# Performance work log

Hardware: AMD Instinct MI355X
Metric: run time of the kernel (lower is better)

Reference implementation:

```python
import jax, jax.numpy as jnp
import numpy as np

B, V, C1, C2 = 4, 256, 64, 32
H0, H1, H2, OUT = 128, 128, 256, 1


def setup_inputs() -> dict:
    key = jax.random.key(0)
    ks = jax.random.split(key, 16)
    init = lambda k, shape: (jax.random.normal(k, shape, jnp.float32) * 0.05)
    return {
        "adjacency": jax.random.randint(ks[0], (B, V, V), 0, 2, jnp.int32),
        "node_features": jax.random.normal(ks[1], (B, V, C1), jnp.float32),
        "edge_attributes": jax.random.normal(ks[2], (B, V, V, C2), jnp.float32),
        # EdgeConvE #1: MLP on concat(x_i, x_j - x_i, e_ij) -> H0 -> H0
        "ec1_W1": init(ks[3], (2 * C1 + C2, H0)), "ec1_b1": jnp.zeros((H0,), jnp.float32),
        "ec1_W2": init(ks[4], (H0, H0)), "ec1_b2": jnp.zeros((H0,), jnp.float32),
        # EdgeConvE #2: input features now H0-dim -> H1 -> H0
        "ec2_W1": init(ks[5], (2 * H0 + C2, H1)), "ec2_b1": jnp.zeros((H1,), jnp.float32),
        "ec2_W2": init(ks[6], (H1, H0)), "ec2_b2": jnp.zeros((H0,), jnp.float32),
        # pair-scoring MLP: Dense(H2, relu) -> Dense(1, sigmoid)
        "h3_W": init(ks[7], (2 * H0, H2)), "h3_b": jnp.zeros((H2,), jnp.float32),
        "out_W": init(ks[8], (H2, OUT)), "out_b": jnp.zeros((OUT,), jnp.float32),
    }


def _edge_conv_e(adj, x, e, W1, b1, W2, b2):
    # EdgeConv with edge attributes: msg_ij = MLP([x_i, x_j - x_i, e_ij]),
    # masked-max aggregation over neighbors j given by adjacency.
    Bv, Vn, C = x.shape
    xi = jnp.broadcast_to(x[:, :, None, :], (Bv, Vn, Vn, C))  # center i
    xj = jnp.broadcast_to(x[:, None, :, :], (Bv, Vn, Vn, C))  # neighbor j
    h = jnp.concatenate([xi, xj - xi, e], axis=-1)            # (B,V,V,2C+Ce)
    h = jax.nn.relu(h @ W1 + b1)
    h = jax.nn.relu(h @ W2 + b2)                               # (B,V,V,H)
    h = jnp.where(adj[..., None] > 0, h, jnp.float32(-1e9))
    out = jnp.max(h, axis=2)                                   # (B,V,H)
    return jnp.where(out <= -1e9, 0.0, out)                    # isolated nodes -> 0


def _feat_concat(x):
    # flat index i*V + j holds [x_j, x_i] (matches tf.repeat axis-0 / axis-1 trick)
    Bv, Vn, C = x.shape
    src = jnp.broadcast_to(x[:, None, :, :], (Bv, Vn, Vn, C)).reshape(Bv, Vn * Vn, C)
    tgt = jnp.broadcast_to(x[:, :, None, :], (Bv, Vn, Vn, C)).reshape(Bv, Vn * Vn, C)
    return jnp.concatenate([src, tgt], axis=-1)                # (B,V*V,2C)


def reference(adjacency, node_features, edge_attributes,
              ec1_W1, ec1_b1, ec1_W2, ec1_b2,
              ec2_W1, ec2_b1, ec2_W2, ec2_b2,
              h3_W, h3_b, out_W, out_b):
    x = _edge_conv_e(adjacency, node_features, edge_attributes, ec1_W1, ec1_b1, ec1_W2, ec1_b2)
    x = _edge_conv_e(adjacency, x, edge_attributes, ec2_W1, ec2_b1, ec2_W2, ec2_b2)
    f = _feat_concat(x)                                        # (B,V*V,2H0)
    f = jax.nn.relu(f @ h3_W + h3_b)
    f = jax.nn.sigmoid(f @ out_W + out_b)                      # (B,V*V,1)
    Bv, Vn, _ = node_features.shape
    return f.reshape(Bv, Vn, Vn)
```

## Files before the change

### kernel.cpp

```cpp
#include <hip/hip_runtime.h>
#include <math.h>

#define B_  4
#define V_  256
#define C1_ 64
#define C2_ 32
#define H0_ 128
#define H2_ 256

typedef short bf16x8 __attribute__((ext_vector_type(8)));
typedef float f32x4  __attribute__((ext_vector_type(4)));

static __device__ __forceinline__ short f2bf(float f) {
    unsigned u = __float_as_uint(f);
    u += 0x7fffu + ((u >> 16) & 1u);
    return (short)(u >> 16);
}

__global__ __launch_bounds__(256) void prep_k(
    const float* __restrict__ W1c1, const float* __restrict__ W21,
    const float* __restrict__ W1c2, const float* __restrict__ W22,
    short* __restrict__ wsW)
{
    int idx = blockIdx.x * 256 + threadIdx.x;
    if (idx < 4096) {
        int n = idx >> 5, k = idx & 31;
        wsW[idx] = f2bf(W1c1[k * H0_ + n]);
    } else if (idx < 20480) {
        int t = idx - 4096; int n = t >> 7, k = t & 127;
        wsW[idx] = f2bf(W21[k * H0_ + n]);
    } else if (idx < 24576) {
        int t = idx - 20480; int n = t >> 5, k = t & 31;
        wsW[idx] = f2bf(W1c2[k * H0_ + n]);
    } else if (idx < 40960) {
        int t = idx - 24576; int n = t >> 7, k = t & 127;
        wsW[idx] = f2bf(W22[k * H0_ + n]);
    }
}

template <int CIN>
__global__ __launch_bounds__(128) void node_pre_k(
    const float* __restrict__ x, const float* __restrict__ W1,
    const float* __restrict__ b1, float* __restrict__ P, float* __restrict__ Q)
{
    const int bi = blockIdx.x, n = threadIdx.x;
    __shared__ __align__(16) float s_x[CIN];
    if (n < CIN) s_x[n] = x[bi * CIN + n];
    __syncthreads();
    float accP = b1[n], accQ = 0.f;
    #pragma unroll 4
    for (int k = 0; k < CIN; k += 4) {
        float4 xv = *reinterpret_cast<const float4*>(&s_x[k]);
        float wa0 = W1[(k + 0) * H0_ + n], wb0 = W1[(CIN + k + 0) * H0_ + n];
        float wa1 = W1[(k + 1) * H0_ + n], wb1 = W1[(CIN + k + 1) * H0_ + n];
        float wa2 = W1[(k + 2) * H0_ + n], wb2 = W1[(CIN + k + 2) * H0_ + n];
        float wa3 = W1[(k + 3) * H0_ + n], wb3 = W1[(CIN + k + 3) * H0_ + n];
        accP = fmaf(xv.x, wa0 - wb0, accP);  accQ = fmaf(xv.x, wb0, accQ);
        accP = fmaf(xv.y, wa1 - wb1, accP);  accQ = fmaf(xv.y, wb1, accQ);
        accP = fmaf(xv.z, wa2 - wb2, accP);  accQ = fmaf(xv.z, wb2, accQ);
        accP = fmaf(xv.w, wa3 - wb3, accP);  accQ = fmaf(xv.w, wb3, accQ);
    }
    P[bi * H0_ + n] = accP;
    Q[bi * H0_ + n] = accQ;
}

__global__ __launch_bounds__(256, 4) void conv_mfma_k(
    const int* __restrict__ adj, const float* __restrict__ e,
    const float* __restrict__ P, const float* __restrict__ Q,
    const short* __restrict__ W1cT, const short* __restrict__ W2T,
    const float* __restrict__ b2, float* __restrict__ out)
{
    const int bi   = blockIdx.x;
    const int b    = bi >> 8;
    const int tid  = threadIdx.x;
    const int w    = tid >> 6;
    const int lane = tid & 63;
    const int l15  = lane & 15;
    const int quad = lane >> 4;

    __shared__ int s_list[V_];
    __shared__ int s_wc[4];
    __shared__ __align__(16) short s_h1[64][136];

    const int av = adj[bi * V_ + tid];
    unsigned long long bm = __ballot(av > 0);
    if (lane == 0) s_wc[w] = __popcll(bm);
    __syncthreads();
    const int cnt = s_wc[0] + s_wc[1] + s_wc[2] + s_wc[3];
    if (av > 0) {
        int base = 0;
        #pragma unroll
        for (int k = 0; k < 4; ++k) if (k < w) base += s_wc[k];
        int pos = base + __popcll(bm & ((1ull << lane) - 1ull));
        s_list[pos] = tid;
    }
    __syncthreads();
    if (cnt == 0) { if (tid < H0_) out[bi * H0_ + tid] = 0.f; return; }

    bf16x8 B2[2][4];
    float bb[2], vmax[2];
    #pragma unroll
    for (int h = 0; h < 2; ++h) {
        const int nt = w * 2 + h;
        #pragma unroll
        for (int kk = 0; kk < 4; ++kk)
            B2[h][kk] = *(const bf16x8*)(W2T + (nt * 16 + l15) * H0_ + kk * 32 + quad * 8);
        bb[h]   = b2[nt * 16 + l15];
        vmax[h] = 0.f;
    }
    float Pp[8];
    #pragma unroll
    for (int nt = 0; nt < 8; ++nt) Pp[nt] = P[bi * H0_ + nt * 16 + l15];

    const int row0 = w * 16;

    int ta0 = row0 + l15; if (ta0 >= cnt) ta0 = cnt - 1;
    const float* er0 = e + (bi * V_ + s_list[ta0]) * C2_ + quad * 8;
    float4 e0 = *(const float4*)(er0);
    float4 e1 = *(const float4*)(er0 + 4);

    for (int t0 = 0; t0 < cnt; t0 += 64) {
        const int tb = t0 + row0;

        bf16x8 A1;
        A1[0] = f2bf(e0.x); A1[1] = f2bf(e0.y); A1[2] = f2bf(e0.z); A1[3] = f2bf(e0.w);
        A1[4] = f2bf(e1.x); A1[5] = f2bf(e1.y); A1[6] = f2bf(e1.z); A1[7] = f2bf(e1.w);

        {
            int tn = t0 + 64 + row0 + l15; if (tn >= cnt) tn = cnt - 1;
            const float* ern = e + (bi * V_ + s_list[tn]) * C2_ + quad * 8;
            e0 = *(const float4*)(ern);
            e1 = *(const float4*)(ern + 4);
        }

        f32x4 acc[8];
        #pragma unroll
        for (int nt = 0; nt < 8; ++nt) {
            bf16x8 B1 = *(const bf16x8*)(W1cT + (nt * 16 + l15) * C2_ + quad * 8);
            f32x4 z = {0.f, 0.f, 0.f, 0.f};
            acc[nt] = __builtin_amdgcn_mfma_f32_16x16x32_bf16(A1, B1, z, 0, 0, 0);
        }

        if (t0 > 0) __syncthreads();

        #pragma unroll
        for (int r = 0; r < 4; ++r) {
            int t = tb + quad * 4 + r; if (t >= cnt) t = cnt - 1;
            const float* Qr = Q + (b * V_ + s_list[t]) * H0_ + l15;
            short* dst = &s_h1[row0 + quad * 4 + r][l15];
            #pragma unroll
            for (int nt = 0; nt < 8; ++nt) {
                float v = acc[nt][r] + Pp[nt] + Qr[nt * 16];
                dst[nt * 16] = f2bf(fmaxf(v, 0.f));
            }
        }

        __syncthreads();

        #pragma unroll
        for (int mt = 0; mt < 4; ++mt) {
            f32x4 a20 = {0.f,0.f,0.f,0.f}, a21 = {0.f,0.f,0.f,0.f};
            #pragma unroll
            for (int kk = 0; kk < 4; ++kk) {
                bf16x8 A2 = *(const bf16x8*)(&s_h1[mt * 16 + l15][kk * 32 + quad * 8]);
                a20 = __builtin_amdgcn_mfma_f32_16x16x32_bf16(A2, B2[0][kk], a20, 0, 0, 0);
                a21 = __builtin_amdgcn_mfma_f32_16x16x32_bf16(A2, B2[1][kk], a21, 0, 0, 0);
            }
            float m0 = fmaxf(fmaxf(a20[0], a20[1]), fmaxf(a20[2], a20[3]));
            float m1 = fmaxf(fmaxf(a21[0], a21[1]), fmaxf(a21[2], a21[3]));
            vmax[0] = fmaxf(vmax[0], fmaxf(m0 + bb[0], 0.f));
            vmax[1] = fmaxf(vmax[1], fmaxf(m1 + bb[1], 0.f));
        }
    }

    #pragma unroll
    for (int h = 0; h < 2; ++h) {
        float p = vmax[h];
        p = fmaxf(p, __shfl_xor(p, 16, 64));
        p = fmaxf(p, __shfl_xor(p, 32, 64));
        if (quad == 0) out[bi * H0_ + (w * 2 + h) * 16 + l15] = p;
    }
}

__global__ __launch_bounds__(256) void pair_pre_k(
    const float* __restrict__ x2, const float* __restrict__ W3,
    const float* __restrict__ b3, float* __restrict__ Ai, float* __restrict__ Aj)
{
    const int bi = blockIdx.x, n = threadIdx.x;
    __shared__ __align__(16) float s_x[H0_];
    if (n < H0_) s_x[n] = x2[bi * H0_ + n];
    __syncthreads();
    float aI = b3[n], aJ = 0.f;
    #pragma unroll 4
    for (int k = 0; k < H0_; k += 4) {
        float4 xv = *reinterpret_cast<const float4*>(&s_x[k]);
        aJ = fmaf(xv.x, W3[(k + 0) * H2_ + n], aJ);
        aJ = fmaf(xv.y, W3[(k + 1) * H2_ + n], aJ);
        aJ = fmaf(xv.z, W3[(k + 2) * H2_ + n], aJ);
        aJ = fmaf(xv.w, W3[(k + 3) * H2_ + n], aJ);
        aI = fmaf(xv.x, W3[(H0_ + k + 0) * H2_ + n], aI);
        aI = fmaf(xv.y, W3[(H0_ + k + 1) * H2_ + n], aI);
        aI = fmaf(xv.z, W3[(H0_ + k + 2) * H2_ + n], aI);
        aI = fmaf(xv.w, W3[(H0_ + k + 3) * H2_ + n], aI);
    }
    Ai[bi * H2_ + n] = aI;
    Aj[bi * H2_ + n] = aJ;
}

__global__ __launch_bounds__(256) void pair_out_k(
    const float* __restrict__ Ai, const float* __restrict__ Aj,
    const float* __restrict__ Wo, const float* __restrict__ bo,
    float* __restrict__ out)
{
    const int blk  = blockIdx.x;
    const int b    = blk >> 9;
    const int ig   = (blk >> 3) & 63;
    const int jq   = blk & 7;
    const int i    = (ig << 2) + (threadIdx.x >> 6);
    const int lane = threadIdx.x & 63;
    const int jj   = lane >> 4;
    const int c    = lane & 15;

    __shared__ __align__(16) float4 s_aj[32 * 64];

    const float4* src = (const float4*)(Aj + (b * V_ + jq * 32) * H2_);
    #pragma unroll
    for (int k = 0; k < 8; ++k) {
        int g  = threadIdx.x + k * 256;
        int jr = g >> 6, f = g & 63;
        s_aj[jr * 64 + (f ^ (jr & 7))] = src[g];
    }

    const float* ai = Ai + (b * V_ + i) * H2_ + c * 16;
    float4 a0 = *(const float4*)(ai);
    float4 a1 = *(const float4*)(ai + 4);
    float4 a2 = *(const float4*)(ai + 8);
    float4 a3 = *(const float4*)(ai + 12);
    const float* wo = Wo + c * 16;
    float4 w0 = *(const float4*)(wo);
    float4 w1 = *(const float4*)(wo + 4);
    float4 w2 = *(const float4*)(wo + 8);
    float4 w3 = *(const float4*)(wo + 12);
    const float bo0 = bo[0];

    __syncthreads();

    for (int js = 0; js < 32; js += 4) {
        const int jr = js + jj;
        const float4* arow = &s_aj[jr * 64];
        const int sw = jr & 7, f0 = c * 4;
        float4 q0 = arow[(f0 + 0) ^ sw];
        float4 q1 = arow[(f0 + 1) ^ sw];
        float4 q2 = arow[(f0 + 2) ^ sw];
        float4 q3 = arow[(f0 + 3) ^ sw];
        float p;
        p = fmaxf(a0.x + q0.x, 0.f) * w0.x;
        p = fmaf(fmaxf(a0.y + q0.y, 0.f), w0.y, p);
        p = fmaf(fmaxf(a0.z + q0.z, 0.f), w0.z, p);
        p = fmaf(fmaxf(a0.w + q0.w, 0.f), w0.w, p);
        p = fmaf(fmaxf(a1.x + q1.x, 0.f), w1.x, p);
        p = fmaf(fmaxf(a1.y + q1.y, 0.f), w1.y, p);
        p = fmaf(fmaxf(a1.z + q1.z, 0.f), w1.z, p);
        p = fmaf(fmaxf(a1.w + q1.w, 0.f), w1.w, p);
        p = fmaf(fmaxf(a2.x + q2.x, 0.f), w2.x, p);
        p = fmaf(fmaxf(a2.y + q2.y, 0.f), w2.y, p);
        p = fmaf(fmaxf(a2.z + q2.z, 0.f), w2.z, p);
        p = fmaf(fmaxf(a2.w + q2.w, 0.f), w2.w, p);
        p = fmaf(fmaxf(a3.x + q3.x, 0.f), w3.x, p);
        p = fmaf(fmaxf(a3.y + q3.y, 0.f), w3.y, p);
        p = fmaf(fmaxf(a3.z + q3.z, 0.f), w3.z, p);
        p = fmaf(fmaxf(a3.w + q3.w, 0.f), w3.w, p);
        #pragma unroll
        for (int off = 1; off < 16; off <<= 1)
            p += __shfl_xor(p, off, 64);
        if (c == 0)
            out[(b * V_ + i) * V_ + jq * 32 + jr] =
                1.f / (1.f + __builtin_expf(-(p + bo0)));
    }
}

extern "C" void kernel_launch(void* const* d_in, const int* in_sizes, int n_in,
                              void* d_out, int out_size, void* d_ws, size_t ws_size,
                              hipStream_t stream) {
    const int*   adj   = (const int*)  d_in[0];
    const float* xf    = (const float*)d_in[1];
    const float* ea    = (const float*)d_in[2];
    const float* ec1W1 = (const float*)d_in[3];
    const float* ec1b1 = (const float*)d_in[4];
    const float* ec1W2 = (const float*)d_in[5];
    const float* ec1b2 = (const float*)d_in[6];
    const float* ec2W1 = (const float*)d_in[7];
    const float* ec2b1 = (const float*)d_in[8];
    const float* ec2W2 = (const float*)d_in[9];
    const float* ec2b2 = (const float*)d_in[10];
    const float* h3W   = (const float*)d_in[11];
    const float* h3b   = (const float*)d_in[12];
    const float* oW    = (const float*)d_in[13];
    const float* ob    = (const float*)d_in[14];
    float* out = (float*)d_out;

    const int NV = B_ * V_;
    float* x1 = (float*)d_ws;
    float* x2 = x1 + NV * H0_;
    float* R  = x2 + NV * H0_;
    float* P  = R;
    float* Q  = R + NV * H0_;
    float* Ai = R;
    float* Aj = R + NV * H2_;
    short* wsW = (short*)(R + 2 * NV * H2_);
    short* W1cT1 = wsW;
    short* W2T1  = wsW + 4096;
    short* W1cT2 = wsW + 20480;
    short* W2T2  = wsW + 24576;

    prep_k<<<160, 256, 0, stream>>>(ec1W1 + 2 * C1_ * H0_, ec1W2,
                                    ec2W1 + 2 * H0_ * H0_, ec2W2, wsW);
    node_pre_k<C1_><<<NV, 128, 0, stream>>>(xf, ec1W1, ec1b1, P, Q);
    conv_mfma_k<<<NV, 256, 0, stream>>>(adj, ea, P, Q, W1cT1, W2T1, ec1b2, x1);
    node_pre_k<H0_><<<NV, 128, 0, stream>>>(x1, ec2W1, ec2b1, P, Q);
    conv_mfma_k<<<NV, 256, 0, stream>>>(adj, ea, P, Q, W1cT2, W2T2, ec2b2, x2);
    pair_pre_k<<<NV, 256, 0, stream>>>(x2, h3W, h3b, Ai, Aj);
    pair_out_k<<<2048, 256, 0, stream>>>(Ai, Aj, oW, ob, out);
}
```

Before: 189.8 us.

## Fuse weight prep with first node precompute and process two nodes per block

Merges the bf16 weight-transpose kernel with the first per-node P/Q precompute into a single launch, which removes one kernel launch. The per-node precompute kernels now use 256-thread blocks that handle two nodes each. The pair precompute kernel computes two nodes per block so each W3 load is reused twice. The aim is to cut launch overhead and global weight-load traffic in these small kernels. The cost is more register pressure and fewer blocks.

```diff
diff --git a/kernel.cpp b/kernel.cpp
--- a/kernel.cpp
+++ b/kernel.cpp
@@ -17,12 +17,11 @@
     return (short)(u >> 16);
 }
 
-__global__ __launch_bounds__(256) void prep_k(
-    const float* __restrict__ W1c1, const float* __restrict__ W21,
+static __device__ __forceinline__ void prep_body(
+    int idx, const float* __restrict__ W1c1, const float* __restrict__ W21,
     const float* __restrict__ W1c2, const float* __restrict__ W22,
     short* __restrict__ wsW)
 {
-    int idx = blockIdx.x * 256 + threadIdx.x;
     if (idx < 4096) {
         int n = idx >> 5, k = idx & 31;
         wsW[idx] = f2bf(W1c1[k * H0_ + n]);
@@ -39,18 +38,22 @@
 }
 
 template <int CIN>
-__global__ __launch_bounds__(128) void node_pre_k(
-    const float* __restrict__ x, const float* __restrict__ W1,
-    const float* __restrict__ b1, float* __restrict__ P, float* __restrict__ Q)
-{
-    const int bi = blockIdx.x, n = threadIdx.x;
-    __shared__ __align__(16) float s_x[CIN];
-    if (n < CIN) s_x[n] = x[bi * CIN + n];
+static __device__ __forceinline__ void npre_body(
+    int node0, const float* __restrict__ x, const float* __restrict__ W1,
+    const float* __restrict__ b1, float* __restrict__ P, float* __restrict__ Q,
+    float* __restrict__ sx2)
+{
+    const int tid  = threadIdx.x;
+    const int half = tid >> 7;
+    const int n    = tid & 127;
+    const int bi   = node0 + half;
+    float* sx = sx2 + half * CIN;
+    if (n < CIN) sx[n] = x[bi * CIN + n];
     __syncthreads();
     float accP = b1[n], accQ = 0.f;
     #pragma unroll 4
     for (int k = 0; k < CIN; k += 4) {
-        float4 xv = *reinterpret_cast<const float4*>(&s_x[k]);
+        float4 xv = *reinterpret_cast<const float4*>(&sx[k]);
         float wa0 = W1[(k + 0) * H0_ + n], wb0 = W1[(CIN + k + 0) * H0_ + n];
         float wa1 = W1[(k + 1) * H0_ + n], wb1 = W1[(CIN + k + 1) * H0_ + n];
         float wa2 = W1[(k + 2) * H0_ + n], wb2 = W1[(CIN + k + 2) * H0_ + n];
@@ -62,6 +65,30 @@
     }
     P[bi * H0_ + n] = accP;
     Q[bi * H0_ + n] = accQ;
+}
+
+__global__ __launch_bounds__(256) void pre1_fused_k(
+    const float* __restrict__ W1c1, const float* __restrict__ W21,
+    const float* __restrict__ W1c2, const float* __restrict__ W22,
+    short* __restrict__ wsW,
+    const float* __restrict__ xf, const float* __restrict__ ec1W1,
+    const float* __restrict__ ec1b1, float* __restrict__ P, float* __restrict__ Q)
+{
+    if (blockIdx.x < 160) {
+        prep_body(blockIdx.x * 256 + threadIdx.x, W1c1, W21, W1c2, W22, wsW);
+    } else {
+        __shared__ __align__(16) float sx2[2 * C1_];
+        npre_body<C1_>((blockIdx.x - 160) * 2, xf, ec1W1, ec1b1, P, Q, sx2);
+    }
+}
+
+template <int CIN>
+__global__ __launch_bounds__(256) void npre2_k(
+    const float* __restrict__ x, const float* __restrict__ W1,
+    const float* __restrict__ b1, float* __restrict__ P, float* __restrict__ Q)
+{
+    __shared__ __align__(16) float sx2[2 * CIN];
+    npre_body<CIN>(blockIdx.x * 2, x, W1, b1, P, Q, sx2);
 }
 
 __global__ __launch_bounds__(256, 4) void conv_mfma_k(
@@ -182,29 +209,43 @@
     }
 }
 
-__global__ __launch_bounds__(256) void pair_pre_k(
+__global__ __launch_bounds__(256) void ppre2_k(
     const float* __restrict__ x2, const float* __restrict__ W3,
     const float* __restrict__ b3, float* __restrict__ Ai, float* __restrict__ Aj)
 {
-    const int bi = blockIdx.x, n = threadIdx.x;
-    __shared__ __align__(16) float s_x[H0_];
-    if (n < H0_) s_x[n] = x2[bi * H0_ + n];
-    __syncthreads();
-    float aI = b3[n], aJ = 0.f;
+    const int nb = blockIdx.x;
+    const int n  = threadIdx.x;
+    __shared__ __align__(16) float s_x[2 * H0_];
+    s_x[n] = x2[nb * 2 * H0_ + n];
+    __syncthreads();
+    const float bv = b3[n];
+    float aI0 = bv, aJ0 = 0.f, aI1 = bv, aJ1 = 0.f;
     #pragma unroll 4
     for (int k = 0; k < H0_; k += 4) {
-        float4 xv = *reinterpret_cast<const float4*>(&s_x[k]);
-        aJ = fmaf(xv.x, W3[(k + 0) * H2_ + n], aJ);
-        aJ = fmaf(xv.y, W3[(k + 1) * H2_ + n], aJ);
-        aJ = fmaf(xv.z, W3[(k + 2) * H2_ + n], aJ);
-        aJ = fmaf(xv.w, W3[(k + 3) * H2_ + n], aJ);
-        aI = fmaf(xv.x, W3[(H0_ + k + 0) * H2_ + n], aI);
-        aI = fmaf(xv.y, W3[(H0_ + k + 1) * H2_ + n], aI);
-        aI = fmaf(xv.z, W3[(H0_ + k + 2) * H2_ + n], aI);
-        aI = fmaf(xv.w, W3[(H0_ + k + 3) * H2_ + n], aI);
-    }
-    Ai[bi * H2_ + n] = aI;
-    Aj[bi * H2_ + n] = aJ;
+        float4 x0 = *reinterpret_cast<const float4*>(&s_x[k]);
+        float4 x1 = *reinterpret_cast<const float4*>(&s_x[H0_ + k]);
+        float wj0 = W3[(k + 0) * H2_ + n];
+        float wj1 = W3[(k + 1) * H2_ + n];
+        float wj2 = W3[(k + 2) * H2_ + n];
+        float wj3 = W3[(k + 3) * H2_ + n];
+        float wi0 = W3[(H0_ + k + 0) * H2_ + n];
+        float wi1 = W3[(H0_ + k + 1) * H2_ + n];
+        float wi2 = W3[(H0_ + k + 2) * H2_ + n];
+        float wi3 = W3[(H0_ + k + 3) * H2_ + n];
+        aJ0 = fmaf(x0.x, wj0, aJ0); aJ0 = fmaf(x0.y, wj1, aJ0);
+        aJ0 = fmaf(x0.z, wj2, aJ0); aJ0 = fmaf(x0.w, wj3, aJ0);
+        aI0 = fmaf(x0.x, wi0, aI0); aI0 = fmaf(x0.y, wi1, aI0);
+        aI0 = fmaf(x0.z, wi2, aI0); aI0 = fmaf(x0.w, wi3, aI0);
+        aJ1 = fmaf(x1.x, wj0, aJ1); aJ1 = fmaf(x1.y, wj1, aJ1);
+        aJ1 = fmaf(x1.z, wj2, aJ1); aJ1 = fmaf(x1.w, wj3, aJ1);
+        aI1 = fmaf(x1.x, wi0, aI1); aI1 = fmaf(x1.y, wi1, aI1);
+        aI1 = fmaf(x1.z, wi2, aI1); aI1 = fmaf(x1.w, wi3, aI1);
+    }
+    const int r0 = nb * 2;
+    Ai[r0 * H2_ + n]       = aI0;
+    Aj[r0 * H2_ + n]       = aJ0;
+    Ai[(r0 + 1) * H2_ + n] = aI1;
+    Aj[(r0 + 1) * H2_ + n] = aJ1;
 }
 
 __global__ __launch_bounds__(256) void pair_out_k(
@@ -313,12 +354,12 @@
     short* W1cT2 = wsW + 20480;
     short* W2T2  = wsW + 24576;
 
-    prep_k<<<160, 256, 0, stream>>>(ec1W1 + 2 * C1_ * H0_, ec1W2,
-                                    ec2W1 + 2 * H0_ * H0_, ec2W2, wsW);
-    node_pre_k<C1_><<<NV, 128, 0, stream>>>(xf, ec1W1, ec1b1, P, Q);
+    pre1_fused_k<<<672, 256, 0, stream>>>(ec1W1 + 2 * C1_ * H0_, ec1W2,
+                                          ec2W1 + 2 * H0_ * H0_, ec2W2, wsW,
+                                          xf, ec1W1, ec1b1, P, Q);
     conv_mfma_k<<<NV, 256, 0, stream>>>(adj, ea, P, Q, W1cT1, W2T1, ec1b2, x1);
-    node_pre_k<H0_><<<NV, 128, 0, stream>>>(x1, ec2W1, ec2b1, P, Q);
+    npre2_k<H0_><<<512, 256, 0, stream>>>(x1, ec2W1, ec2b1, P, Q);
     conv_mfma_k<<<NV, 256, 0, stream>>>(adj, ea, P, Q, W1cT2, W2T2, ec2b2, x2);
-    pair_pre_k<<<NV, 256, 0, stream>>>(x2, h3W, h3b, Ai, Aj);
+    ppre2_k<<<512, 256, 0, stream>>>(x2, h3W, h3b, Ai, Aj);
     pair_out_k<<<2048, 256, 0, stream>>>(Ai, Aj, oW, ob, out);
 }
```

Result: faster. 185.6 us (-2.2%).

## Fuse node pre-transforms into conv kernels and merge weight prep launches

Applied to the files above, without the earlier changes.

Weight conversion and the first node pre-transform now share one launch, with each pre-transform block covering two nodes. Each EdgeConv kernel keeps its aggregated node vector in shared memory and computes the next stage's per-node projections itself (P/Q for conv2, Ai/Aj for pair scoring). This cuts seven launches to four and removes the global write and re-read of the x1/x2 intermediates. In exchange, each conv block does extra serial matvec work at its end, and the fused kernels may carry more register and shared-memory pressure.

```diff
diff --git a/kernel.cpp b/kernel.cpp
--- a/kernel.cpp
+++ b/kernel.cpp
@@ -17,12 +17,11 @@
     return (short)(u >> 16);
 }
 
-__global__ __launch_bounds__(256) void prep_k(
-    const float* __restrict__ W1c1, const float* __restrict__ W21,
+static __device__ __forceinline__ void prep_body(
+    int idx, const float* __restrict__ W1c1, const float* __restrict__ W21,
     const float* __restrict__ W1c2, const float* __restrict__ W22,
     short* __restrict__ wsW)
 {
-    int idx = blockIdx.x * 256 + threadIdx.x;
     if (idx < 4096) {
         int n = idx >> 5, k = idx & 31;
         wsW[idx] = f2bf(W1c1[k * H0_ + n]);
@@ -39,18 +38,22 @@
 }
 
 template <int CIN>
-__global__ __launch_bounds__(128) void node_pre_k(
-    const float* __restrict__ x, const float* __restrict__ W1,
-    const float* __restrict__ b1, float* __restrict__ P, float* __restrict__ Q)
-{
-    const int bi = blockIdx.x, n = threadIdx.x;
-    __shared__ __align__(16) float s_x[CIN];
-    if (n < CIN) s_x[n] = x[bi * CIN + n];
+static __device__ __forceinline__ void npre_body(
+    int node0, const float* __restrict__ x, const float* __restrict__ W1,
+    const float* __restrict__ b1, float* __restrict__ P, float* __restrict__ Q,
+    float* __restrict__ sx2)
+{
+    const int tid  = threadIdx.x;
+    const int half = tid >> 7;
+    const int n    = tid & 127;
+    const int bi   = node0 + half;
+    float* sx = sx2 + half * CIN;
+    if (n < CIN) sx[n] = x[bi * CIN + n];
     __syncthreads();
     float accP = b1[n], accQ = 0.f;
     #pragma unroll 4
     for (int k = 0; k < CIN; k += 4) {
-        float4 xv = *reinterpret_cast<const float4*>(&s_x[k]);
+        float4 xv = *reinterpret_cast<const float4*>(&sx[k]);
         float wa0 = W1[(k + 0) * H0_ + n], wb0 = W1[(CIN + k + 0) * H0_ + n];
         float wa1 = W1[(k + 1) * H0_ + n], wb1 = W1[(CIN + k + 1) * H0_ + n];
         float wa2 = W1[(k + 2) * H0_ + n], wb2 = W1[(CIN + k + 2) * H0_ + n];
@@ -64,13 +67,29 @@
     Q[bi * H0_ + n] = accQ;
 }
 
-__global__ __launch_bounds__(256, 4) void conv_mfma_k(
-    const int* __restrict__ adj, const float* __restrict__ e,
+__global__ __launch_bounds__(256) void pre1_fused_k(
+    const float* __restrict__ W1c1, const float* __restrict__ W21,
+    const float* __restrict__ W1c2, const float* __restrict__ W22,
+    short* __restrict__ wsW,
+    const float* __restrict__ xf, const float* __restrict__ ec1W1,
+    const float* __restrict__ ec1b1, float* __restrict__ P, float* __restrict__ Q)
+{
+    if (blockIdx.x < 160) {
+        prep_body(blockIdx.x * 256 + threadIdx.x, W1c1, W21, W1c2, W22, wsW);
+    } else {
+        __shared__ __align__(16) float sx2[2 * C1_];
+        npre_body<C1_>((blockIdx.x - 160) * 2, xf, ec1W1, ec1b1, P, Q, sx2);
+    }
+}
+
+static __device__ void conv_core(
+    const int bi, const int* __restrict__ adj, const float* __restrict__ e,
     const float* __restrict__ P, const float* __restrict__ Q,
     const short* __restrict__ W1cT, const short* __restrict__ W2T,
-    const float* __restrict__ b2, float* __restrict__ out)
-{
-    const int bi   = blockIdx.x;
+    const float* __restrict__ b2,
+    int* __restrict__ s_list, int* __restrict__ s_wc, short (*s_h1)[136],
+    float* __restrict__ s_x)
+{
     const int b    = bi >> 8;
     const int tid  = threadIdx.x;
     const int w    = tid >> 6;
@@ -78,10 +97,6 @@
     const int l15  = lane & 15;
     const int quad = lane >> 4;
 
-    __shared__ int s_list[V_];
-    __shared__ int s_wc[4];
-    __shared__ __align__(16) short s_h1[64][136];
-
     const int av = adj[bi * V_ + tid];
     unsigned long long bm = __ballot(av > 0);
     if (lane == 0) s_wc[w] = __popcll(bm);
@@ -95,7 +110,7 @@
         s_list[pos] = tid;
     }
     __syncthreads();
-    if (cnt == 0) { if (tid < H0_) out[bi * H0_ + tid] = 0.f; return; }
+    if (cnt == 0) { if (tid < H0_) s_x[tid] = 0.f; return; }
 
     bf16x8 B2[2][4];
     float bb[2], vmax[2];
@@ -178,18 +193,81 @@
         float p = vmax[h];
         p = fmaxf(p, __shfl_xor(p, 16, 64));
         p = fmaxf(p, __shfl_xor(p, 32, 64));
-        if (quad == 0) out[bi * H0_ + (w * 2 + h) * 16 + l15] = p;
-    }
-}
-
-__global__ __launch_bounds__(256) void pair_pre_k(
-    const float* __restrict__ x2, const float* __restrict__ W3,
-    const float* __restrict__ b3, float* __restrict__ Ai, float* __restrict__ Aj)
-{
-    const int bi = blockIdx.x, n = threadIdx.x;
+        if (quad == 0) s_x[(w * 2 + h) * 16 + l15] = p;
+    }
+}
+
+__global__ __launch_bounds__(256, 4) void conv1_fused_k(
+    const int* __restrict__ adj, const float* __restrict__ e,
+    const float* __restrict__ P, const float* __restrict__ Q,
+    const short* __restrict__ W1cT, const short* __restrict__ W2T,
+    const float* __restrict__ b2,
+    const float* __restrict__ W1n, const float* __restrict__ b1n,
+    float* __restrict__ P2, float* __restrict__ Q2)
+{
+    const int bi = blockIdx.x;
+    __shared__ int s_list[V_];
+    __shared__ int s_wc[4];
+    __shared__ __align__(16) short s_h1[64][136];
     __shared__ __align__(16) float s_x[H0_];
-    if (n < H0_) s_x[n] = x2[bi * H0_ + n];
-    __syncthreads();
+
+    conv_core(bi, adj, e, P, Q, W1cT, W2T, b2, s_list, s_wc, s_h1, s_x);
+    __syncthreads();
+
+    const int tid  = threadIdx.x;
+    const int half = tid >> 7;
+    const int n    = tid & 127;
+    if (half == 0) {
+        float accP = b1n[n];
+        #pragma unroll 4
+        for (int k = 0; k < H0_; k += 4) {
+            float4 xv = *reinterpret_cast<const float4*>(&s_x[k]);
+            float wa0 = W1n[(k + 0) * H0_ + n], wb0 = W1n[(H0_ + k + 0) * H0_ + n];
+            float wa1 = W1n[(k + 1) * H0_ + n], wb1 = W1n[(H0_ + k + 1) * H0_ + n];
+            float wa2 = W1n[(k + 2) * H0_ + n], wb2 = W1n[(H0_ + k + 2) * H0_ + n];
+            float wa3 = W1n[(k + 3) * H0_ + n], wb3 = W1n[(H0_ + k + 3) * H0_ + n];
+            accP = fmaf(xv.x, wa0 - wb0, accP);
+            accP = fmaf(xv.y, wa1 - wb1, accP);
+            accP = fmaf(xv.z, wa2 - wb2, accP);
+            accP = fmaf(xv.w, wa3 - wb3, accP);
+        }
+        P2[bi * H0_ + n] = accP;
+    } else {
+        float accQ = 0.f;
+        #pragma unroll 4
+        for (int k = 0; k < H0_; k += 4) {
+            float4 xv = *reinterpret_cast<const float4*>(&s_x[k]);
+            float wb0 = W1n[(H0_ + k + 0) * H0_ + n];
+            float wb1 = W1n[(H0_ + k + 1) * H0_ + n];
+            float wb2 = W1n[(H0_ + k + 2) * H0_ + n];
+            float wb3 = W1n[(H0_ + k + 3) * H0_ + n];
+            accQ = fmaf(xv.x, wb0, accQ);
+            accQ = fmaf(xv.y, wb1, accQ);
+            accQ = fmaf(xv.z, wb2, accQ);
+            accQ = fmaf(xv.w, wb3, accQ);
+        }
+        Q2[bi * H0_ + n] = accQ;
+    }
+}
+
+__global__ __launch_bounds__(256, 4) void conv2_fused_k(
+    const int* __restrict__ adj, const float* __restrict__ e,
+    const float* __restrict__ P, const float* __restrict__ Q,
+    const short* __restrict__ W1cT, const short* __restrict__ W2T,
+    const float* __restrict__ b2,
+    const float* __restrict__ W3, const float* __restrict__ b3,
+    float* __restrict__ Ai, float* __restrict__ Aj)
+{
+    const int bi = blockIdx.x;
+    __shared__ int s_list[V_];
+    __shared__ int s_wc[4];
+    __shared__ __align__(16) short s_h1[64][136];
+    __shared__ __align__(16) float s_x[H0_];
+
+    conv_core(bi, adj, e, P, Q, W1cT, W2T, b2, s_list, s_wc, s_h1, s_x);
+    __syncthreads();
+
+    const int n = threadIdx.x;
     float aI = b3[n], aJ = 0.f;
     #pragma unroll 4
     for (int k = 0; k < H0_; k += 4) {
@@ -300,25 +378,24 @@
     float* out = (float*)d_out;
 
     const int NV = B_ * V_;
-    float* x1 = (float*)d_ws;
-    float* x2 = x1 + NV * H0_;
-    float* R  = x2 + NV * H0_;
-    float* P  = R;
-    float* Q  = R + NV * H0_;
-    float* Ai = R;
-    float* Aj = R + NV * H2_;
-    short* wsW = (short*)(R + 2 * NV * H2_);
+    float* P  = (float*)d_ws;
+    float* Q  = P  + NV * H0_;
+    float* P2 = Q  + NV * H0_;
+    float* Q2 = P2 + NV * H0_;
+    float* Ai = Q2 + NV * H0_;
+    float* Aj = Ai + NV * H2_;
+    short* wsW = (short*)(Aj + NV * H2_);
     short* W1cT1 = wsW;
     short* W2T1  = wsW + 4096;
     short* W1cT2 = wsW + 20480;
     short* W2T2  = wsW + 24576;
 
-    prep_k<<<160, 256, 0, stream>>>(ec1W1 + 2 * C1_ * H0_, ec1W2,
-                                    ec2W1 + 2 * H0_ * H0_, ec2W2, wsW);
-    node_pre_k<C1_><<<NV, 128, 0, stream>>>(xf, ec1W1, ec1b1, P, Q);
-    conv_mfma_k<<<NV, 256, 0, stream>>>(adj, ea, P, Q, W1cT1, W2T1, ec1b2, x1);
-    node_pre_k<H0_><<<NV, 128, 0, stream>>>(x1, ec2W1, ec2b1, P, Q);
-    conv_mfma_k<<<NV, 256, 0, stream>>>(adj, ea, P, Q, W1cT2, W2T2, ec2b2, x2);
-    pair_pre_k<<<NV, 256, 0, stream>>>(x2, h3W, h3b, Ai, Aj);
+    pre1_fused_k<<<672, 256, 0, stream>>>(ec1W1 + 2 * C1_ * H0_, ec1W2,
+                                          ec2W1 + 2 * H0_ * H0_, ec2W2, wsW,
+                                          xf, ec1W1, ec1b1, P, Q);
+    conv1_fused_k<<<NV, 256, 0, stream>>>(adj, ea, P, Q, W1cT1, W2T1, ec1b2,
+                                          ec2W1, ec2b1, P2, Q2);
+    conv2_fused_k<<<NV, 256, 0, stream>>>(adj, ea, P2, Q2, W1cT2, W2T2, ec2b2,
+                                          h3W, h3b, Ai, Aj);
     pair_out_k<<<2048, 256, 0, stream>>>(Ai, Aj, oW, ob, out);
 }
```

Result: slower. 300.9 us (+58.5%).
